# Optimization experiments

Measured on AMD Instinct MI355X. Metric: run time of the kernel, lower is better.

## Reference

```python
import jax, jax.numpy as jnp
import numpy as np

N_STATES = 25
N_CHANNELS = 80
BATCH = 64
TIME = 400


def setup_inputs() -> dict:
    key = jax.random.key(0)
    k1, k2, k3 = jax.random.split(key, 3)
    alpha_t = jax.random.uniform(k1, (BATCH, TIME, N_STATES), dtype=jnp.float32)
    mu = jax.random.normal(k2, (N_STATES, N_CHANNELS), dtype=jnp.float32)
    D = jax.random.normal(k3, (N_STATES, N_CHANNELS, N_CHANNELS), dtype=jnp.float32)
    # Keras initializer: Constant(log(e - 1)) so softplus(alpha_scaling) == 1 at init
    alpha_scaling = jnp.full((N_STATES,), np.log(np.e - 1.0), dtype=jnp.float32)
    return {"alpha_t": alpha_t, "mu": mu, "D": D, "alpha_scaling": alpha_scaling}


def reference(alpha_t, mu, D, alpha_scaling):
    # a: [batch, time, n_states], scaled per-state by softplus(alpha_scaling)
    a = alpha_t * jax.nn.softplus(alpha_scaling)
    # m_t = sum_j a_jt mu_j  -> [batch, time, channels]
    m_t = jnp.einsum("btj,jc->btc", a, mu)
    # C_t = sum_j a_jt D_j   -> [batch, time, channels, channels]
    C_t = jnp.einsum("btj,jcd->btcd", a, D)
    return (m_t, C_t)
```

## Files before the change

kernel.cpp:

```cpp
#include <hip/hip_runtime.h>
#include <math.h>

#define BATCH 64
#define TIME 400
#define BT (BATCH * TIME)
#define S 25
#define CH 80
#define CD (CH * CH)

#define BT_TILE 32
#define CD_TILE 512
#define NTHREADS 256

__global__ void scale_kernel(const float* __restrict__ alpha_scaling,
                             float* __restrict__ scale) {
    int k = threadIdx.x;
    if (k < S) {
        float x = alpha_scaling[k];
        scale[k] = fmaxf(x, 0.0f) + log1pf(expf(-fabsf(x)));
    }
}

__global__ __launch_bounds__(NTHREADS) void m_kernel(
    const float* __restrict__ alpha, const float* __restrict__ mu,
    const float* __restrict__ scale, float* __restrict__ out_m) {
    __shared__ float s_mu[S * CH];
    __shared__ float s_scale[S];
    for (int i = threadIdx.x; i < S * CH; i += NTHREADS) s_mu[i] = mu[i];
    if (threadIdx.x < S) s_scale[threadIdx.x] = scale[threadIdx.x];
    __syncthreads();

    int i4 = blockIdx.x * NTHREADS + threadIdx.x;
    const int total4 = BT * CH / 4;
    if (i4 >= total4) return;
    int e = i4 * 4;
    int bt = e / CH;
    int c = e - bt * CH;
    const float* arow = alpha + (size_t)bt * S;
    float4 acc = {0.f, 0.f, 0.f, 0.f};
#pragma unroll
    for (int k = 0; k < S; k++) {
        float a = arow[k] * s_scale[k];
        float4 m4 = *(const float4*)&s_mu[k * CH + c];
        acc.x += a * m4.x;
        acc.y += a * m4.y;
        acc.z += a * m4.z;
        acc.w += a * m4.w;
    }
    *(float4*)&out_m[e] = acc;
}

__global__ __launch_bounds__(NTHREADS) void c_kernel(
    const float* __restrict__ alpha, const float* __restrict__ D,
    const float* __restrict__ scale, float* __restrict__ out_c) {
    __shared__ float s_D[S * CD_TILE];
    __shared__ float s_a[S * BT_TILE];

    const int cd0 = blockIdx.x * CD_TILE;
    const int bt0 = blockIdx.y * BT_TILE;
    const int vcols = min(CD_TILE, CD - cd0);
    const int tid = threadIdx.x;

    for (int i = tid; i < S * BT_TILE; i += NTHREADS) {
        int row = i / S;
        int k = i - row * S;
        s_a[k * BT_TILE + row] = alpha[(size_t)(bt0 + row) * S + k] * scale[k];
    }
    const int nf4 = S * (CD_TILE / 4);
    for (int i = tid; i < nf4; i += NTHREADS) {
        int k = i >> 7;
        int col = (i & 127) * 4;
        if (col < vcols) {
            float4 v = *(const float4*)&D[(size_t)k * CD + cd0 + col];
            *(float4*)&s_D[k * CD_TILE + col] = v;
        }
    }
    __syncthreads();

    const int c0 = 2 * tid;
    float acc0[BT_TILE];
    float acc1[BT_TILE];
#pragma unroll
    for (int r = 0; r < BT_TILE; r++) {
        acc0[r] = 0.f;
        acc1[r] = 0.f;
    }

#pragma unroll 5
    for (int k = 0; k < S; k++) {
        float d0 = s_D[k * CD_TILE + c0];
        float d1 = s_D[k * CD_TILE + c0 + 1];
        const float4* a4 = (const float4*)&s_a[k * BT_TILE];
#pragma unroll
        for (int r4 = 0; r4 < BT_TILE / 4; r4++) {
            float4 av = a4[r4];
            acc0[4 * r4 + 0] += av.x * d0;
            acc1[4 * r4 + 0] += av.x * d1;
            acc0[4 * r4 + 1] += av.y * d0;
            acc1[4 * r4 + 1] += av.y * d1;
            acc0[4 * r4 + 2] += av.z * d0;
            acc1[4 * r4 + 2] += av.z * d1;
            acc0[4 * r4 + 3] += av.w * d0;
            acc1[4 * r4 + 3] += av.w * d1;
        }
    }

    if (c0 < vcols) {
#pragma unroll
        for (int r = 0; r < BT_TILE; r++) {
            float2 v = {acc0[r], acc1[r]};
            *(float2*)&out_c[(size_t)(bt0 + r) * CD + cd0 + c0] = v;
        }
    }
}

extern "C" void kernel_launch(void* const* d_in, const int* in_sizes, int n_in,
                              void* d_out, int out_size, void* d_ws, size_t ws_size,
                              hipStream_t stream) {
    const float* alpha = (const float*)d_in[0];
    const float* mu = (const float*)d_in[1];
    const float* D = (const float*)d_in[2];
    const float* alpha_scaling = (const float*)d_in[3];

    float* out = (float*)d_out;
    float* out_m = out;
    float* out_c = out + BT * CH;
    float* scale = (float*)d_ws;

    scale_kernel<<<1, 64, 0, stream>>>(alpha_scaling, scale);

    const int total4 = BT * CH / 4;
    m_kernel<<<(total4 + NTHREADS - 1) / NTHREADS, NTHREADS, 0, stream>>>(
        alpha, mu, scale, out_m);

    dim3 grid((CD + CD_TILE - 1) / CD_TILE, BT / BT_TILE);
    c_kernel<<<grid, NTHREADS, 0, stream>>>(alpha, D, scale, out_c);
}
```

Measured before the change: 796.0 us.

## Keep scaled D in registers and stream alpha rows without shared memory

The C kernel drops its shared-memory staging of D and alpha. Each thread now loads its two D columns across all states into registers, pre-multiplied by the softplus scale, then loops over 64 batch-time rows reading alpha directly from global memory (wave-uniform, so cached/scalar) and writing one float2 per row. This removes the block barrier, the LDS traffic and the large accumulator arrays, which should raise occupancy for a store-bandwidth-bound kernel. The cost is that alpha is reread from cache by every thread and each row's result is stored right after it is computed.

```diff
diff --git a/kernel.cpp b/kernel.cpp
--- a/kernel.cpp
+++ b/kernel.cpp
@@ -8,9 +8,9 @@
 #define CH 80
 #define CD (CH * CH)
 
-#define BT_TILE 32
-#define CD_TILE 512
 #define NTHREADS 256
+#define CD_TILE (2 * NTHREADS)
+#define ROWS 64
 
 __global__ void scale_kernel(const float* __restrict__ alpha_scaling,
                              float* __restrict__ scale) {
@@ -53,64 +53,35 @@
 __global__ __launch_bounds__(NTHREADS) void c_kernel(
     const float* __restrict__ alpha, const float* __restrict__ D,
     const float* __restrict__ scale, float* __restrict__ out_c) {
-    __shared__ float s_D[S * CD_TILE];
-    __shared__ float s_a[S * BT_TILE];
+    const int cd0 = blockIdx.x * CD_TILE;
+    const int bt0 = blockIdx.y * ROWS;
+    const int vcols = min(CD_TILE, CD - cd0);
+    const int c0 = 2 * (int)threadIdx.x;
+    if (c0 >= vcols) return;
 
-    const int cd0 = blockIdx.x * CD_TILE;
-    const int bt0 = blockIdx.y * BT_TILE;
-    const int vcols = min(CD_TILE, CD - cd0);
-    const int tid = threadIdx.x;
-
-    for (int i = tid; i < S * BT_TILE; i += NTHREADS) {
-        int row = i / S;
-        int k = i - row * S;
-        s_a[k * BT_TILE + row] = alpha[(size_t)(bt0 + row) * S + k] * scale[k];
-    }
-    const int nf4 = S * (CD_TILE / 4);
-    for (int i = tid; i < nf4; i += NTHREADS) {
-        int k = i >> 7;
-        int col = (i & 127) * 4;
-        if (col < vcols) {
-            float4 v = *(const float4*)&D[(size_t)k * CD + cd0 + col];
-            *(float4*)&s_D[k * CD_TILE + col] = v;
-        }
-    }
-    __syncthreads();
-
-    const int c0 = 2 * tid;
-    float acc0[BT_TILE];
-    float acc1[BT_TILE];
+    float d0[S], d1[S];
 #pragma unroll
-    for (int r = 0; r < BT_TILE; r++) {
-        acc0[r] = 0.f;
-        acc1[r] = 0.f;
+    for (int k = 0; k < S; ++k) {
+        float sc = scale[k];
+        float2 dv = *(const float2*)&D[(size_t)k * CD + cd0 + c0];
+        d0[k] = dv.x * sc;
+        d1[k] = dv.y * sc;
     }
 
-#pragma unroll 5
-    for (int k = 0; k < S; k++) {
-        float d0 = s_D[k * CD_TILE + c0];
-        float d1 = s_D[k * CD_TILE + c0 + 1];
-        const float4* a4 = (const float4*)&s_a[k * BT_TILE];
+    const float* arow = alpha + (size_t)bt0 * S;
+    float* crow = out_c + (size_t)bt0 * CD + cd0 + c0;
+    for (int r = 0; r < ROWS; ++r) {
+        float acc0 = 0.f, acc1 = 0.f;
 #pragma unroll
-        for (int r4 = 0; r4 < BT_TILE / 4; r4++) {
-            float4 av = a4[r4];
-            acc0[4 * r4 + 0] += av.x * d0;
-            acc1[4 * r4 + 0] += av.x * d1;
-            acc0[4 * r4 + 1] += av.y * d0;
-            acc1[4 * r4 + 1] += av.y * d1;
-            acc0[4 * r4 + 2] += av.z * d0;
-            acc1[4 * r4 + 2] += av.z * d1;
-            acc0[4 * r4 + 3] += av.w * d0;
-            acc1[4 * r4 + 3] += av.w * d1;
+        for (int k = 0; k < S; ++k) {
+            float a = arow[k];
+            acc0 = fmaf(a, d0[k], acc0);
+            acc1 = fmaf(a, d1[k], acc1);
         }
-    }
-
-    if (c0 < vcols) {
-#pragma unroll
-        for (int r = 0; r < BT_TILE; r++) {
-            float2 v = {acc0[r], acc1[r]};
-            *(float2*)&out_c[(size_t)(bt0 + r) * CD + cd0 + c0] = v;
-        }
+        float2 v = {acc0, acc1};
+        *(float2*)crow = v;
+        arow += S;
+        crow += CD;
     }
 }
 
@@ -133,6 +104,6 @@
     m_kernel<<<(total4 + NTHREADS - 1) / NTHREADS, NTHREADS, 0, stream>>>(
         alpha, mu, scale, out_m);
 
-    dim3 grid((CD + CD_TILE - 1) / CD_TILE, BT / BT_TILE);
+    dim3 grid((CD + CD_TILE - 1) / CD_TILE, BT / ROWS);
     c_kernel<<<grid, NTHREADS, 0, stream>>>(alpha, D, scale, out_c);
 }
```

Result: faster. 721.3 us (-9.4%).
